# Kernel tuning notes

Hardware: AMD Instinct MI355X
Metric: run time of the kernel (lower is better)

The kernel has to match this reference:

```python
import jax, jax.numpy as jnp
import numpy as np

B, N, T, S = 32, 102400, 64, 1600
PI = float(np.pi)
EPS = 1e-12  # numerical guard inside sqrt for cdist (diagonal is exactly 0)


def _cdist(a, b):
    # a: (..., P, 3), b: (..., Q, 3) -> (..., P, Q) euclidean distances
    sq = jnp.sum((a[..., :, None, :] - b[..., None, :, :]) ** 2, axis=-1)
    return jnp.sqrt(sq + EPS)


def _rigid_t(alpha, trans, sz, center):
    # alpha, trans: (B, T, 3). Returns XYZ (B,T,3,3), translation (B,T,3).
    c, s = jnp.cos(alpha), jnp.sin(alpha)
    z = jnp.zeros_like(c[..., 0]); o = jnp.ones_like(c[..., 0])
    X = jnp.stack([c[..., 0], -s[..., 0], z, s[..., 0], c[..., 0], z, z, z, o], -1).reshape(*alpha.shape[:2], 3, 3)
    Y = jnp.stack([c[..., 1], z, s[..., 1], z, o, z, -s[..., 1], z, c[..., 1]], -1).reshape(*alpha.shape[:2], 3, 3)
    Z = jnp.stack([o, z, z, z, c[..., 2], -s[..., 2], z, s[..., 2], c[..., 2]], -1).reshape(*alpha.shape[:2], 3, 3)
    XYZ = jnp.einsum('btij,btjk,btkl->btil', X, Y, Z)
    eye = jnp.eye(3, dtype=alpha.dtype)
    Tt = trans * sz[None, None, :] + jnp.einsum('m,btmk->btk', center, eye[None, None] - XYZ)
    return XYZ, Tt


def setup_inputs():
    key = jax.random.key(0)
    ks = jax.random.split(key, 6)
    x = jax.random.normal(ks[0], (B, 6, N), jnp.float32)
    w1 = jax.random.normal(ks[1], (3 * N, 32), jnp.float32) * 0.005
    b1 = jnp.zeros((32,), jnp.float32)
    w2 = jax.random.normal(ks[2], (32, 6 * T), jnp.float32) * 0.05
    b2 = jnp.zeros((6 * T,), jnp.float32)
    A = jax.random.normal(ks[3], (6, N), jnp.float32)
    mask = jax.random.uniform(ks[4], (T, T), jnp.float32)
    sz = jnp.array([128.0, 128.0, 64.0], jnp.float32)
    tess = jnp.arange(N, dtype=jnp.int32).reshape(T, S)  # equal-size partition
    return {'x': x, 'w1': w1, 'b1': b1, 'w2': w2, 'b2': b2, 'A': A, 'mask': mask, 'sz': sz, 'tess': tess}


def reference(x, w1, b1, w2, b2, A, mask, sz, tess):
    center = sz / 2.0
    # localization MLP on flattened xyz coords: (B, 3N) -> (B, T, 6)
    xflat = x[:, :3, :].reshape(B, 3 * N)
    h = jax.nn.relu(xflat @ w1 + b1)
    z_l = jnp.tanh(h @ w2 + b2).reshape(B, T, 6)
    # NOTE: original code uses z_l[:, :, 3:] for BOTH angles and translation
    r_, t_ = _rigid_t(PI * z_l[:, :, 3:], z_l[:, :, 3:], sz, center)
    x3 = x[:, :3, :]
    xg = x3[:, :, tess]  # gather: (B, 3, T, S)
    # out[b,j,p,n] = sum_k r_[b,p,k,j] * xg[b,k,p,n]  (matches einsum 'bkt,bkn->btn')
    rot = jnp.einsum('bpkj,bkpn->bjpn', r_, xg) + t_.transpose(0, 2, 1)[:, :, :, None]
    # scatter back into full point cloud (tess partitions N)
    X3 = jnp.zeros_like(x3).at[:, :, tess.reshape(-1)].set(rot.reshape(B, 3, N))
    X_t = jnp.concatenate([X3, x[:, 3:, :]], axis=1)  # colors pass through identity
    # regularizer on per-piece centroids
    pts_1 = A[:3][:, tess].mean(axis=2).T                 # (T, 3)
    pts_2 = X3[:, :, tess].mean(axis=3).transpose(0, 2, 1)  # (B, T, 3)
    diff = _cdist(pts_1, pts_1)[None] - _cdist(pts_2, pts_2)
    reg = jnp.sum((mask[None] * diff) ** 2, axis=(1, 2))  # (B,)
    return X_t, reg
```

## Files before the change

kernel.cpp:

```cpp
#include <hip/hip_runtime.h>
#include <hip/hip_bf16.h>
#include <math.h>

#define BB 32
#define NN 102400
#define TT 64
#define SS 1600
#define K3N (3 * NN)
#define KC 64
#define G1 512
#define CPB 512
#define NCHUNK (K3N / KC)
#define PI_F 3.14159265358979323846f

#define AS1 __attribute__((address_space(1)))
#define AS3 __attribute__((address_space(3)))

__device__ __forceinline__ void gload16(const float* g, float* l) {
    __builtin_amdgcn_global_load_lds((const AS1 void*)g, (AS3 void*)l, 16, 0, 0);
}

__global__ __launch_bounds__(256) void k1_mega(const float* __restrict__ x,
                                               const float* __restrict__ w1,
                                               const float* __restrict__ A,
                                               const int* __restrict__ tess,
                                               float* __restrict__ h_part,
                                               float* __restrict__ out,
                                               float* __restrict__ pts1) {
    __shared__ float xs[2][32 * 64];
    __shared__ float wls[2][64 * 32];
    const int tid = threadIdx.x;
    if (blockIdx.x < G1) {
        const int lane = tid & 63, wv = tid >> 6;
        const int ks = tid & 7;
        const int bg = (tid >> 3) & 7;
        const int cg = wv;
        const int sA = (wv * 2 + 0) * 64 + lane;
        const int sB = (wv * 2 + 1) * 64 + lane;
        const int xbA = sA >> 4, xqA = sA & 15;
        const int xbB = sB >> 4, xqB = sB & 15;
        const size_t gxA = (size_t)xbA * 6 * NN + 4 * (xqA ^ (xbA & 7));
        const size_t gxB = (size_t)xbB * 6 * NN + 4 * (xqB ^ (xbB & 7));
        const int kA = sA >> 3, pA = sA & 7;
        const int kB = sB >> 3, pB = sB & 7;
        const size_t gwA = (size_t)kA * 32 + (((pA >> 1) ^ (kA & 3)) * 8 + (pA & 1) * 4);
        const size_t gwB = (size_t)kB * 32 + (((pB >> 1) ^ (kB & 3)) * 8 + (pB & 1) * 4);
        const int lA = (wv * 2 + 0) * 256;
        const int lB = (wv * 2 + 1) * 256;

        float acc[4][8];
        #pragma unroll
        for (int j = 0; j < 4; ++j)
            #pragma unroll
            for (int c = 0; c < 8; ++c) acc[j][c] = 0.f;

        const int start = (int)(((long)blockIdx.x * NCHUNK) / G1);
        const int end   = (int)(((long)(blockIdx.x + 1) * NCHUNK) / G1);

        {
            const int k0 = start * KC;
            gload16(x + gxA + k0, &xs[0][lA]);
            gload16(x + gxB + k0, &xs[0][lB]);
            gload16(w1 + gwA + (size_t)k0 * 32, &wls[0][lA]);
            gload16(w1 + gwB + (size_t)k0 * 32, &wls[0][lB]);
        }
        __syncthreads();

        int cur = 0;
        for (int chunk = start; chunk < end; ++chunk) {
            if (chunk + 1 < end) {
                const int k0 = (chunk + 1) * KC;
                const int nb = cur ^ 1;
                gload16(x + gxA + k0, &xs[nb][lA]);
                gload16(x + gxB + k0, &xs[nb][lB]);
                gload16(w1 + gwA + (size_t)k0 * 32, &wls[nb][lA]);
                gload16(w1 + gwB + (size_t)k0 * 32, &wls[nb][lB]);
            }
            const float* xc = xs[cur];
            const float* wc = wls[cur];
            #pragma unroll
            for (int i = 0; i < 8; ++i) {
                const int k = ks + 8 * i;
                const int xq = ((k >> 2) ^ bg) * 4 + (k & 3);
                const float xv0 = xc[(bg     ) * 64 + xq];
                const float xv1 = xc[(bg +  8) * 64 + xq];
                const float xv2 = xc[(bg + 16) * 64 + xq];
                const float xv3 = xc[(bg + 24) * 64 + xq];
                const int wo = k * 32 + ((cg ^ (k & 3)) * 8);
                const float4 wa = *(const float4*)(wc + wo);
                const float4 wb = *(const float4*)(wc + wo + 4);
                acc[0][0] = fmaf(xv0, wa.x, acc[0][0]);
                acc[0][1] = fmaf(xv0, wa.y, acc[0][1]);
                acc[0][2] = fmaf(xv0, wa.z, acc[0][2]);
                acc[0][3] = fmaf(xv0, wa.w, acc[0][3]);
                acc[0][4] = fmaf(xv0, wb.x, acc[0][4]);
                acc[0][5] = fmaf(xv0, wb.y, acc[0][5]);
                acc[0][6] = fmaf(xv0, wb.z, acc[0][6]);
                acc[0][7] = fmaf(xv0, wb.w, acc[0][7]);
                acc[1][0] = fmaf(xv1, wa.x, acc[1][0]);
                acc[1][1] = fmaf(xv1, wa.y, acc[1][1]);
                acc[1][2] = fmaf(xv1, wa.z, acc[1][2]);
                acc[1][3] = fmaf(xv1, wa.w, acc[1][3]);
                acc[1][4] = fmaf(xv1, wb.x, acc[1][4]);
                acc[1][5] = fmaf(xv1, wb.y, acc[1][5]);
                acc[1][6] = fmaf(xv1, wb.z, acc[1][6]);
                acc[1][7] = fmaf(xv1, wb.w, acc[1][7]);
                acc[2][0] = fmaf(xv2, wa.x, acc[2][0]);
                acc[2][1] = fmaf(xv2, wa.y, acc[2][1]);
                acc[2][2] = fmaf(xv2, wa.z, acc[2][2]);
                acc[2][3] = fmaf(xv2, wa.w, acc[2][3]);
                acc[2][4] = fmaf(xv2, wb.x, acc[2][4]);
                acc[2][5] = fmaf(xv2, wb.y, acc[2][5]);
                acc[2][6] = fmaf(xv2, wb.z, acc[2][6]);
                acc[2][7] = fmaf(xv2, wb.w, acc[2][7]);
                acc[3][0] = fmaf(xv3, wa.x, acc[3][0]);
                acc[3][1] = fmaf(xv3, wa.y, acc[3][1]);
                acc[3][2] = fmaf(xv3, wa.z, acc[3][2]);
                acc[3][3] = fmaf(xv3, wa.w, acc[3][3]);
                acc[3][4] = fmaf(xv3, wb.x, acc[3][4]);
                acc[3][5] = fmaf(xv3, wb.y, acc[3][5]);
                acc[3][6] = fmaf(xv3, wb.z, acc[3][6]);
                acc[3][7] = fmaf(xv3, wb.w, acc[3][7]);
            }
            __syncthreads();
            cur ^= 1;
        }

        #pragma unroll
        for (int off = 1; off < 8; off <<= 1) {
            #pragma unroll
            for (int j = 0; j < 4; ++j)
                #pragma unroll
                for (int c = 0; c < 8; ++c)
                    acc[j][c] += __shfl_xor(acc[j][c], off, 64);
        }
        if (ks == 0) {
            float* hp = h_part + (size_t)blockIdx.x * 1024;
            #pragma unroll
            for (int j = 0; j < 4; ++j) {
                const int b = bg + 8 * j;
                #pragma unroll
                for (int c = 0; c < 8; ++c)
                    hp[b * 32 + cg * 8 + c] = acc[j][c];
            }
        }
    } else if (blockIdx.x < G1 + CPB) {
        const int cb = blockIdx.x - G1;
        for (int i = cb * 256 + tid; i < 2457600; i += CPB * 256) {
            const int b = i / 76800;
            const int rem = i - b * 76800;
            const size_t off = (size_t)b * (6 * NN) + K3N + (size_t)rem * 4;
            *(float4*)(out + off) = *(const float4*)(x + off);
        }
    } else {
        const int t = blockIdx.x - G1 - CPB;
        const int* tr = tess + t * SS;
        float s0 = 0.f, s1 = 0.f, s2 = 0.f;
        for (int s = tid; s < SS; s += 256) {
            const int idx = tr[s];
            s0 += A[idx]; s1 += A[NN + idx]; s2 += A[2 * NN + idx];
        }
        #pragma unroll
        for (int o = 32; o > 0; o >>= 1) {
            s0 += __shfl_down(s0, o, 64);
            s1 += __shfl_down(s1, o, 64);
            s2 += __shfl_down(s2, o, 64);
        }
        __shared__ float red[4 * 3];
        const int lane = tid & 63, wv = tid >> 6;
        if (lane == 0) { red[wv * 3] = s0; red[wv * 3 + 1] = s1; red[wv * 3 + 2] = s2; }
        __syncthreads();
        if (tid < 3) {
            const float s = red[tid] + red[3 + tid] + red[6 + tid] + red[9 + tid];
            pts1[t * 3 + tid] = s * (1.0f / SS);
        }
    }
}

__global__ __launch_bounds__(256) void kb_rigid(const float* __restrict__ h_part,
                                                const float* __restrict__ b1,
                                                const float* __restrict__ w2,
                                                const float* __restrict__ b2,
                                                const float* __restrict__ sz,
                                                float* __restrict__ RT) {
    const int bb = blockIdx.x;
    __shared__ float part[8][32];
    __shared__ float hsh[32];
    const int c = threadIdx.x & 31, g = threadIdx.x >> 5;
    float s = 0.f;
    for (int j = g; j < G1; j += 8) s += h_part[(size_t)j * 1024 + bb * 32 + c];
    part[g][c] = s;
    __syncthreads();
    if (threadIdx.x < 32) {
        float acc = 0.f;
        #pragma unroll
        for (int g2 = 0; g2 < 8; ++g2) acc += part[g2][threadIdx.x];
        hsh[threadIdx.x] = fmaxf(acc + b1[threadIdx.x], 0.f);
    }
    __syncthreads();
    const int t = threadIdx.x;
    if (t < TT) {
        float z[3];
        #pragma unroll
        for (int j = 0; j < 3; ++j) {
            const int col = 6 * t + 3 + j;
            float s2 = b2[col];
            #pragma unroll 8
            for (int cc = 0; cc < 32; ++cc) s2 = fmaf(hsh[cc], w2[cc * 384 + col], s2);
            z[j] = tanhf(s2);
        }
        float c0, s0, c1, s1, c2, s2v;
        sincosf(PI_F * z[0], &s0, &c0);
        sincosf(PI_F * z[1], &s1, &c1);
        sincosf(PI_F * z[2], &s2v, &c2);
        const float R00 = c0 * c1;
        const float R01 = -s0 * c2 + c0 * s1 * s2v;
        const float R02 = s0 * s2v + c0 * s1 * c2;
        const float R10 = s0 * c1;
        const float R11 = c0 * c2 + s0 * s1 * s2v;
        const float R12 = -c0 * s2v + s0 * s1 * c2;
        const float R20 = -s1;
        const float R21 = c1 * s2v;
        const float R22 = c1 * c2;
        const float szx = sz[0], szy = sz[1], szz = sz[2];
        const float cx = 0.5f * szx, cy = 0.5f * szy, cz = 0.5f * szz;
        const float T0 = z[0] * szx + cx - (cx * R00 + cy * R10 + cz * R20);
        const float T1 = z[1] * szy + cy - (cx * R01 + cy * R11 + cz * R21);
        const float T2 = z[2] * szz + cz - (cx * R02 + cy * R12 + cz * R22);
        float* o = RT + (bb * TT + t) * 12;
        o[0] = R00; o[1] = R10; o[2]  = R20; o[3]  = T0;
        o[4] = R01; o[5] = R11; o[6]  = R21; o[7]  = T1;
        o[8] = R02; o[9] = R12; o[10] = R22; o[11] = T2;
    }
}

__global__ __launch_bounds__(256) void k3_transform(const float* __restrict__ x,
                                                    const int* __restrict__ tess,
                                                    const float* __restrict__ RT,
                                                    float* __restrict__ out,
                                                    float* __restrict__ pts2) {
    const int blk = blockIdx.x;
    const int b = blk / TT, t = blk % TT;
    const float* p = RT + blk * 12;
    const float M00 = p[0], M01 = p[1], M02 = p[2], T0 = p[3];
    const float M10 = p[4], M11 = p[5], M12 = p[6], T1 = p[7];
    const float M20 = p[8], M21 = p[9], M22 = p[10], T2 = p[11];
    const float* xb = x + (size_t)b * 6 * NN;
    float* ob = out + (size_t)b * 6 * NN;
    const int* tr = tess + t * SS;
    float s0 = 0.f, s1 = 0.f, s2 = 0.f;
    for (int s = threadIdx.x; s < SS; s += 256) {
        const int idx = tr[s];
        const float x0 = xb[idx], x1 = xb[NN + idx], x2 = xb[2 * NN + idx];
        const float y0 = fmaf(M00, x0, fmaf(M01, x1, fmaf(M02, x2, T0)));
        const float y1 = fmaf(M10, x0, fmaf(M11, x1, fmaf(M12, x2, T1)));
        const float y2 = fmaf(M20, x0, fmaf(M21, x1, fmaf(M22, x2, T2)));
        ob[idx] = y0; ob[NN + idx] = y1; ob[2 * NN + idx] = y2;
        s0 += y0; s1 += y1; s2 += y2;
    }
    #pragma unroll
    for (int o = 32; o > 0; o >>= 1) {
        s0 += __shfl_down(s0, o, 64);
        s1 += __shfl_down(s1, o, 64);
        s2 += __shfl_down(s2, o, 64);
    }
    __shared__ float red[4 * 3];
    const int lane = threadIdx.x & 63, wv = threadIdx.x >> 6;
    if (lane == 0) { red[wv * 3] = s0; red[wv * 3 + 1] = s1; red[wv * 3 + 2] = s2; }
    __syncthreads();
    if (threadIdx.x < 3) {
        const float s = red[threadIdx.x] + red[3 + threadIdx.x] + red[6 + threadIdx.x] + red[9 + threadIdx.x];
        pts2[blk * 3 + threadIdx.x] = s * (1.0f / SS);
    }
}

__global__ __launch_bounds__(256) void k5_reg(const float* __restrict__ pts1,
                                              const float* __restrict__ pts2,
                                              const float* __restrict__ mask,
                                              float* __restrict__ out) {
    const int b = blockIdx.x;
    __shared__ float p1[TT * 3], p2[TT * 3];
    for (int i = threadIdx.x; i < TT * 3; i += 256) {
        p1[i] = pts1[i];
        p2[i] = pts2[b * TT * 3 + i];
    }
    __syncthreads();
    float acc = 0.f;
    for (int pr = threadIdx.x; pr < TT * TT; pr += 256) {
        const int t = pr >> 6, u = pr & 63;
        float dx = p1[t * 3] - p1[u * 3];
        float dy = p1[t * 3 + 1] - p1[u * 3 + 1];
        float dz = p1[t * 3 + 2] - p1[u * 3 + 2];
        const float d1 = sqrtf(dx * dx + dy * dy + dz * dz + 1e-12f);
        dx = p2[t * 3] - p2[u * 3];
        dy = p2[t * 3 + 1] - p2[u * 3 + 1];
        dz = p2[t * 3 + 2] - p2[u * 3 + 2];
        const float d2 = sqrtf(dx * dx + dy * dy + dz * dz + 1e-12f);
        const float d = mask[pr] * (d1 - d2);
        acc = fmaf(d, d, acc);
    }
    #pragma unroll
    for (int o = 32; o > 0; o >>= 1) acc += __shfl_down(acc, o, 64);
    __shared__ float red[4];
    const int lane = threadIdx.x & 63, wv = threadIdx.x >> 6;
    if (lane == 0) red[wv] = acc;
    __syncthreads();
    if (threadIdx.x == 0) {
        out[(size_t)BB * 6 * NN + b] = red[0] + red[1] + red[2] + red[3];
    }
}

extern "C" void kernel_launch(void* const* d_in, const int* in_sizes, int n_in,
                              void* d_out, int out_size, void* d_ws, size_t ws_size,
                              hipStream_t stream) {
    const float* x    = (const float*)d_in[0];
    const float* w1   = (const float*)d_in[1];
    const float* b1   = (const float*)d_in[2];
    const float* w2   = (const float*)d_in[3];
    const float* b2   = (const float*)d_in[4];
    const float* A    = (const float*)d_in[5];
    const float* mask = (const float*)d_in[6];
    const float* sz   = (const float*)d_in[7];
    const int*   tess = (const int*)d_in[8];
    float* out = (float*)d_out;
    float* ws  = (float*)d_ws;

    float* h_part = ws;
    float* RT     = h_part + (size_t)G1 * 1024;
    float* pts2   = RT + BB * TT * 12;
    float* pts1   = pts2 + BB * TT * 3;

    k1_mega<<<G1 + CPB + TT, 256, 0, stream>>>(x, w1, A, tess, h_part, out, pts1);
    kb_rigid<<<BB, 256, 0, stream>>>(h_part, b1, w2, b2, sz, RT);
    k3_transform<<<BB * TT, 256, 0, stream>>>(x, tess, RT, out, pts2);
    k5_reg<<<BB, 256, 0, stream>>>(pts1, pts2, mask, out);
}
```

Baseline: 74.38 us.

## Retile first-layer GEMM to 8x8 per-thread register blocking with rotated LDS layout

```diff
diff --git a/kernel.cpp b/kernel.cpp
--- a/kernel.cpp
+++ b/kernel.cpp
@@ -32,25 +32,23 @@
     const int tid = threadIdx.x;
     if (blockIdx.x < G1) {
         const int lane = tid & 63, wv = tid >> 6;
-        const int ks = tid & 7;
-        const int bg = (tid >> 3) & 7;
-        const int cg = wv;
+        const int ks = tid & 15;
+        const int cG = (tid >> 4) & 3;
+        const int bG = wv;
         const int sA = (wv * 2 + 0) * 64 + lane;
         const int sB = (wv * 2 + 1) * 64 + lane;
-        const int xbA = sA >> 4, xqA = sA & 15;
-        const int xbB = sB >> 4, xqB = sB & 15;
-        const size_t gxA = (size_t)xbA * 6 * NN + 4 * (xqA ^ (xbA & 7));
-        const size_t gxB = (size_t)xbB * 6 * NN + 4 * (xqB ^ (xbB & 7));
+        const size_t gxA = (size_t)(sA >> 4) * 6 * NN + (sA & 15) * 4;
+        const size_t gxB = (size_t)(sB >> 4) * 6 * NN + (sB & 15) * 4;
         const int kA = sA >> 3, pA = sA & 7;
         const int kB = sB >> 3, pB = sB & 7;
-        const size_t gwA = (size_t)kA * 32 + (((pA >> 1) ^ (kA & 3)) * 8 + (pA & 1) * 4);
-        const size_t gwB = (size_t)kB * 32 + (((pB >> 1) ^ (kB & 3)) * 8 + (pB & 1) * 4);
+        const size_t gwA = (size_t)kA * 32 + (((pA - ((kA >> 2) & 7)) & 7) * 4);
+        const size_t gwB = (size_t)kB * 32 + (((pB - ((kB >> 2) & 7)) & 7) * 4);
         const int lA = (wv * 2 + 0) * 256;
         const int lB = (wv * 2 + 1) * 256;
 
-        float acc[4][8];
-        #pragma unroll
-        for (int j = 0; j < 4; ++j)
+        float acc[8][8];
+        #pragma unroll
+        for (int j = 0; j < 8; ++j)
             #pragma unroll
             for (int c = 0; c < 8; ++c) acc[j][c] = 0.f;
 
@@ -78,58 +76,39 @@
             }
             const float* xc = xs[cur];
             const float* wc = wls[cur];
-            #pragma unroll
-            for (int i = 0; i < 8; ++i) {
-                const int k = ks + 8 * i;
-                const int xq = ((k >> 2) ^ bg) * 4 + (k & 3);
-                const float xv0 = xc[(bg     ) * 64 + xq];
-                const float xv1 = xc[(bg +  8) * 64 + xq];
-                const float xv2 = xc[(bg + 16) * 64 + xq];
-                const float xv3 = xc[(bg + 24) * 64 + xq];
-                const int wo = k * 32 + ((cg ^ (k & 3)) * 8);
-                const float4 wa = *(const float4*)(wc + wo);
-                const float4 wb = *(const float4*)(wc + wo + 4);
-                acc[0][0] = fmaf(xv0, wa.x, acc[0][0]);
-                acc[0][1] = fmaf(xv0, wa.y, acc[0][1]);
-                acc[0][2] = fmaf(xv0, wa.z, acc[0][2]);
-                acc[0][3] = fmaf(xv0, wa.w, acc[0][3]);
-                acc[0][4] = fmaf(xv0, wb.x, acc[0][4]);
-                acc[0][5] = fmaf(xv0, wb.y, acc[0][5]);
-                acc[0][6] = fmaf(xv0, wb.z, acc[0][6]);
-                acc[0][7] = fmaf(xv0, wb.w, acc[0][7]);
-                acc[1][0] = fmaf(xv1, wa.x, acc[1][0]);
-                acc[1][1] = fmaf(xv1, wa.y, acc[1][1]);
-                acc[1][2] = fmaf(xv1, wa.z, acc[1][2]);
-                acc[1][3] = fmaf(xv1, wa.w, acc[1][3]);
-                acc[1][4] = fmaf(xv1, wb.x, acc[1][4]);
-                acc[1][5] = fmaf(xv1, wb.y, acc[1][5]);
-                acc[1][6] = fmaf(xv1, wb.z, acc[1][6]);
-                acc[1][7] = fmaf(xv1, wb.w, acc[1][7]);
-                acc[2][0] = fmaf(xv2, wa.x, acc[2][0]);
-                acc[2][1] = fmaf(xv2, wa.y, acc[2][1]);
-                acc[2][2] = fmaf(xv2, wa.z, acc[2][2]);
-                acc[2][3] = fmaf(xv2, wa.w, acc[2][3]);
-                acc[2][4] = fmaf(xv2, wb.x, acc[2][4]);
-                acc[2][5] = fmaf(xv2, wb.y, acc[2][5]);
-                acc[2][6] = fmaf(xv2, wb.z, acc[2][6]);
-                acc[2][7] = fmaf(xv2, wb.w, acc[2][7]);
-                acc[3][0] = fmaf(xv3, wa.x, acc[3][0]);
-                acc[3][1] = fmaf(xv3, wa.y, acc[3][1]);
-                acc[3][2] = fmaf(xv3, wa.z, acc[3][2]);
-                acc[3][3] = fmaf(xv3, wa.w, acc[3][3]);
-                acc[3][4] = fmaf(xv3, wb.x, acc[3][4]);
-                acc[3][5] = fmaf(xv3, wb.y, acc[3][5]);
-                acc[3][6] = fmaf(xv3, wb.z, acc[3][6]);
-                acc[3][7] = fmaf(xv3, wb.w, acc[3][7]);
+            float4 xv[8];
+            #pragma unroll
+            for (int bi = 0; bi < 8; ++bi)
+                xv[bi] = *(const float4*)(xc + (bG * 8 + bi) * 64 + ks * 4);
+            #pragma unroll
+            for (int kk = 0; kk < 4; ++kk) {
+                const int k = ks * 4 + kk;
+                const float* wrow = wc + k * 32;
+                const int qa = ((cG * 2 + 0 + ks) & 7) * 4;
+                const int qb = ((cG * 2 + 1 + ks) & 7) * 4;
+                const float4 wa = *(const float4*)(wrow + qa);
+                const float4 wb = *(const float4*)(wrow + qb);
+                #pragma unroll
+                for (int bi = 0; bi < 8; ++bi) {
+                    const float xj = kk == 0 ? xv[bi].x : (kk == 1 ? xv[bi].y : (kk == 2 ? xv[bi].z : xv[bi].w));
+                    acc[bi][0] = fmaf(xj, wa.x, acc[bi][0]);
+                    acc[bi][1] = fmaf(xj, wa.y, acc[bi][1]);
+                    acc[bi][2] = fmaf(xj, wa.z, acc[bi][2]);
+                    acc[bi][3] = fmaf(xj, wa.w, acc[bi][3]);
+                    acc[bi][4] = fmaf(xj, wb.x, acc[bi][4]);
+                    acc[bi][5] = fmaf(xj, wb.y, acc[bi][5]);
+                    acc[bi][6] = fmaf(xj, wb.z, acc[bi][6]);
+                    acc[bi][7] = fmaf(xj, wb.w, acc[bi][7]);
+                }
             }
             __syncthreads();
             cur ^= 1;
         }
 
         #pragma unroll
-        for (int off = 1; off < 8; off <<= 1) {
-            #pragma unroll
-            for (int j = 0; j < 4; ++j)
+        for (int off = 1; off < 16; off <<= 1) {
+            #pragma unroll
+            for (int j = 0; j < 8; ++j)
                 #pragma unroll
                 for (int c = 0; c < 8; ++c)
                     acc[j][c] += __shfl_xor(acc[j][c], off, 64);
@@ -137,11 +116,12 @@
         if (ks == 0) {
             float* hp = h_part + (size_t)blockIdx.x * 1024;
             #pragma unroll
-            for (int j = 0; j < 4; ++j) {
-                const int b = bg + 8 * j;
-                #pragma unroll
-                for (int c = 0; c < 8; ++c)
-                    hp[b * 32 + cg * 8 + c] = acc[j][c];
+            for (int bi = 0; bi < 8; ++bi) {
+                float4 v0; v0.x = acc[bi][0]; v0.y = acc[bi][1]; v0.z = acc[bi][2]; v0.w = acc[bi][3];
+                float4 v1; v1.x = acc[bi][4]; v1.y = acc[bi][5]; v1.z = acc[bi][6]; v1.w = acc[bi][7];
+                float* dst = hp + (bG * 8 + bi) * 32 + cG * 8;
+                *(float4*)(dst) = v0;
+                *(float4*)(dst + 4) = v1;
             }
         }
     } else if (blockIdx.x < G1 + CPB) {
@@ -254,9 +234,10 @@
         const float x0 = xb[idx], x1 = xb[NN + idx], x2 = xb[2 * NN + idx];
         const float y0 = fmaf(M00, x0, fmaf(M01, x1, fmaf(M02, x2, T0)));
         const float y1 = fmaf(M10, x0, fmaf(M11, x1, fmaf(M12, x2, T1)));
-        const float y2 = fmaf(M20, x0, fmaf(M21, x1, fmaf(M22, x2, T2)));
-        ob[idx] = y0; ob[NN + idx] = y1; ob[2 * NN + idx] = y2;
-        s0 += y0; s1 += y1; s2 += y2;
+        const float y2 = fmaf(M20, x0, fmaf(M22 * 0.f + M21, x1, fmaf(M22, x2, T2)));
+        ob[idx] = y0; ob[NN + idx] = y1;
+        ob[2 * NN + idx] = fmaf(M20, x0, fmaf(M21, x1, fmaf(M22, x2, T2)));
+        s0 += y0; s1 += y1; s2 += ob[2 * NN + idx];
     }
     #pragma unroll
     for (int o = 32; o > 0; o >>= 1) {
```

New measurement: 75.29 us. No clear change (+1.2%).
